# Optimization experiments

Measured on AMD Instinct MI355X. Metric: run time of the kernel, lower is better.

Reference implementation:

```python
import jax, jax.numpy as jnp
import numpy as np

N_NODES = 100000
N_EDGES = 1600000
IN_CH = 64
HID = 64
N_GRAPHS = 64


def _sage_conv(x, src, dst, Wl, bl, Wr, n_nodes):
    # PyG SAGEConv (aggr='mean'): out = lin_l(mean_{j in N(i)} x_j) + lin_r(x_i)
    msg = x[src]                                            # [E, d] gather
    agg = jax.ops.segment_sum(msg, dst, num_segments=n_nodes)
    cnt = jax.ops.segment_sum(jnp.ones((src.shape[0],), x.dtype), dst,
                              num_segments=n_nodes)
    agg = agg / jnp.maximum(cnt, 1.0)[:, None]
    return agg @ Wl + bl + x @ Wr


def setup_inputs() -> dict:
    key = jax.random.key(0)
    ks = jax.random.split(key, 16)
    x = jax.random.normal(ks[0], (N_NODES, IN_CH), jnp.float32)
    edge_index = jax.random.randint(ks[1], (2, N_EDGES), 0, N_NODES, jnp.int64)
    batch = jnp.sort(jax.random.randint(ks[2], (N_NODES,), 0, N_GRAPHS, jnp.int64))

    def glorot(k, fan_in, fan_out):
        s = jnp.sqrt(2.0 / (fan_in + fan_out))
        return jax.random.normal(k, (fan_in, fan_out), jnp.float32) * s

    params = {
        'W1l': glorot(ks[3], IN_CH, HID), 'b1': jnp.zeros((HID,), jnp.float32),
        'W1r': glorot(ks[4], IN_CH, HID),
        'W2l': glorot(ks[5], HID, HID), 'b2': jnp.zeros((HID,), jnp.float32),
        'W2r': glorot(ks[6], HID, HID),
        'W3l': glorot(ks[7], HID, HID), 'b3': jnp.zeros((HID,), jnp.float32),
        'W3r': glorot(ks[8], HID, HID),
        'Wc1': glorot(ks[9], HID, HID // 2), 'bc1': jnp.zeros((HID // 2,), jnp.float32),
        'Wc2': glorot(ks[10], HID // 2, 2), 'bc2': jnp.zeros((2,), jnp.float32),
    }
    return {'x': x, 'edge_index': edge_index, 'batch': batch, **params}


def reference(x, edge_index, batch,
              W1l, b1, W1r, W2l, b2, W2r, W3l, b3, W3r,
              Wc1, bc1, Wc2, bc2):
    src, dst = edge_index[0], edge_index[1]
    n = x.shape[0]
    h = jax.nn.relu(_sage_conv(x, src, dst, W1l, b1, W1r, n))   # dropout = identity (eval)
    h = jax.nn.relu(_sage_conv(h, src, dst, W2l, b2, W2r, n))
    h = jax.nn.relu(_sage_conv(h, src, dst, W3l, b3, W3r, n))
    # global mean pool over graphs
    sums = jax.ops.segment_sum(h, batch, num_segments=N_GRAPHS)
    cnts = jax.ops.segment_sum(jnp.ones((n,), h.dtype), batch, num_segments=N_GRAPHS)
    g = sums / jnp.maximum(cnts, 1.0)[:, None]                  # [G, HID]
    # MLP head (dropout = identity at eval)
    return jax.nn.relu(g @ Wc1 + bc1) @ Wc2 + bc2               # [G, 2]
```

## Files before the change

kernel.cpp:

```cpp
#include <hip/hip_runtime.h>
#include <hip/hip_bf16.h>
#include <hip/hip_fp16.h>

typedef unsigned int u32;
typedef unsigned short u16;
typedef _Float16 f16x8 __attribute__((ext_vector_type(8)));
typedef float f32x4 __attribute__((ext_vector_type(4)));

#define NBLK1 512
#define MMBLK 784

__device__ __forceinline__ u16 f2h(float f) { return __half_as_ushort(__float2half(f)); }
__device__ __forceinline__ u32 packh2(float a, float b) {
    return (u32)f2h(a) | ((u32)f2h(b) << 16);
}
__device__ __forceinline__ __half2 sx(__half2 v, int m) {
    int iv = __shfl_xor(*(int*)&v, m, 64);
    return *(__half2*)&iv;
}

__device__ __forceinline__ int gidx(const void* p, long long i, int w64) {
    if (w64) return (int)((const long long*)p)[i];
    return ((const int*)p)[i];
}

__global__ void init_detect(const int* __restrict__ edge_words, int* __restrict__ flag,
                            u32* __restrict__ ticket, float* __restrict__ pool, int E) {
    const int tid = threadIdx.x;
    for (int i = tid; i < 4096; i += 256) pool[i] = 0.f;
    if (tid == 0) *ticket = 0;
    __shared__ int anyNZ;
    if (tid == 0) anyNZ = 0;
    __syncthreads();
    const long long totalWords = 2LL * E;
    const long long step = totalWords / 1024;
    int nz = 0;
    for (int i = 0; i < 4; ++i) {
        long long w = ((long long)(tid * 4 + i) * step) | 1;
        if (w < totalWords) nz |= edge_words[w];
    }
    if (nz) atomicOr(&anyNZ, 1);
    __syncthreads();
    if (tid == 0) flag[0] = anyNZ ? 0 : 1;
}

__global__ void __launch_bounds__(256) fused_hist_mm1(
        const void* __restrict__ edge, const int* __restrict__ flag,
        u32* __restrict__ HG, int E, int n, int nb1,
        const float* __restrict__ X, const float* __restrict__ Wl,
        const float* __restrict__ Wr, const float* __restrict__ Bv,
        u16* __restrict__ Z, u16* __restrict__ R) {
    if (blockIdx.x < NBLK1) {
        __shared__ u32 h[256];
        const int tid = threadIdx.x;
        h[tid] = 0;
        __syncthreads();
        const int w64 = flag[0];
        const int chunk = (E + NBLK1 - 1) / NBLK1;
        const int s = blockIdx.x * chunk;
        const int e = min(s + chunk, E);
        for (int i = s + tid; i < e; i += 256) {
            int d = gidx(edge, (long long)E + i, w64);
            if ((unsigned)d >= (unsigned)n) d = 0;
            atomicAdd(&h[d >> 9], 1);
        }
        __syncthreads();
        for (int b = tid; b < nb1; b += 256) HG[b * NBLK1 + blockIdx.x] = h[b];
        return;
    }
    const int lane = threadIdx.x & 63;
    const int quad = lane >> 4;
    const int m16 = lane & 15;
    f16x8 bl[2][4], br[2][4];
#pragma unroll
    for (int kh = 0; kh < 2; ++kh)
#pragma unroll
        for (int t = 0; t < 4; ++t)
#pragma unroll
            for (int j = 0; j < 8; ++j) {
                int k = kh * 32 + quad * 8 + j;
                int c = t * 16 + m16;
                bl[kh][t][j] = (_Float16)Wl[k * 64 + c];
                br[kh][t][j] = (_Float16)Wr[k * 64 + c];
            }
    float bias_t[4];
#pragma unroll
    for (int t = 0; t < 4; ++t) bias_t[t] = Bv[t * 16 + m16];

    const int ntiles = (n + 15) >> 4;
    const int nwaves = (gridDim.x - NBLK1) * 4;
    for (int tile = (blockIdx.x - NBLK1) * 4 + (threadIdx.x >> 6); tile < ntiles; tile += nwaves) {
        const int nodeBase = tile << 4;
        int nodeA = nodeBase + m16;
        if (nodeA >= n) nodeA = n - 1;
        f16x8 a[2];
#pragma unroll
        for (int kh = 0; kh < 2; ++kh) {
            const float4* p = (const float4*)(X + (size_t)nodeA * 64 + kh * 32 + quad * 8);
            float4 x0 = p[0], x1 = p[1];
            a[kh][0] = (_Float16)x0.x; a[kh][1] = (_Float16)x0.y;
            a[kh][2] = (_Float16)x0.z; a[kh][3] = (_Float16)x0.w;
            a[kh][4] = (_Float16)x1.x; a[kh][5] = (_Float16)x1.y;
            a[kh][6] = (_Float16)x1.z; a[kh][7] = (_Float16)x1.w;
        }
        f32x4 cl[4], cr[4];
#pragma unroll
        for (int t = 0; t < 4; ++t) {
            f32x4 c0 = {0.f, 0.f, 0.f, 0.f};
            c0 = __builtin_amdgcn_mfma_f32_16x16x32_f16(a[0], bl[0][t], c0, 0, 0, 0);
            c0 = __builtin_amdgcn_mfma_f32_16x16x32_f16(a[1], bl[1][t], c0, 0, 0, 0);
            cl[t] = c0;
            f32x4 c1 = {0.f, 0.f, 0.f, 0.f};
            c1 = __builtin_amdgcn_mfma_f32_16x16x32_f16(a[0], br[0][t], c1, 0, 0, 0);
            c1 = __builtin_amdgcn_mfma_f32_16x16x32_f16(a[1], br[1][t], c1, 0, 0, 0);
            cr[t] = c1;
        }
#pragma unroll
        for (int rg = 0; rg < 4; ++rg) {
            const int node = nodeBase + quad * 4 + rg;
            if (node < n) {
#pragma unroll
                for (int t = 0; t < 4; ++t) {
                    const int c = t * 16 + m16;
                    Z[(size_t)node * 64 + c] = f2h(cl[t][rg]);
                    R[(size_t)node * 64 + c] = f2h(cr[t][rg] + bias_t[t]);
                }
            }
        }
    }
}

__global__ void scanAB(u32* __restrict__ HG, u32* __restrict__ blockSums,
                       u32* __restrict__ SB, u32* __restrict__ ticket, int n) {
    __shared__ u32 ts[256];
    __shared__ int isLast;
    const int ITEMS = 8;
    const int tid = threadIdx.x;
    int base = blockIdx.x * 2048 + tid * ITEMS;
    u32 v[ITEMS];
    u32 sum = 0;
#pragma unroll
    for (int i = 0; i < ITEMS; ++i) {
        int idx = base + i;
        v[i] = (idx < n) ? HG[idx] : 0;
        sum += v[i];
    }
    ts[tid] = sum;
    __syncthreads();
    u32 incl = sum;
    for (int d = 1; d < 256; d <<= 1) {
        u32 y = 0;
        if (tid >= d) y = ts[tid - d];
        __syncthreads();
        incl += y;
        ts[tid] = incl;
        __syncthreads();
    }
    u32 run = incl - sum;
#pragma unroll
    for (int i = 0; i < ITEMS; ++i) {
        int idx = base + i;
        if (idx < n) HG[idx] = run;
        run += v[i];
    }
    if (tid == 255) {
        atomicExch(&blockSums[blockIdx.x], incl);
        __threadfence();
        u32 t = atomicAdd(ticket, 1);
        isLast = (t == gridDim.x - 1);
    }
    __syncthreads();
    if (!isLast) return;
    const int nb = gridDim.x;
    u32 bv = (tid < nb) ? atomicAdd(&blockSums[tid], 0u) : 0;
    ts[tid] = bv;
    __syncthreads();
    u32 bincl = bv;
    for (int d = 1; d < 256; d <<= 1) {
        u32 y = 0;
        if (tid >= d) y = ts[tid - d];
        __syncthreads();
        bincl += y;
        ts[tid] = bincl;
        __syncthreads();
    }
    if (tid < nb) SB[tid] = bincl - bv;
}

__global__ void __launch_bounds__(256) p1_scatter(const void* __restrict__ edge,
                                                  const int* __restrict__ flag,
                                                  const u32* __restrict__ HG,
                                                  const u32* __restrict__ SB,
                                                  u32* __restrict__ P, int E, int n, int nb1) {
    __shared__ u32 base[256];
    __shared__ u32 cur[256];
    const int tid = threadIdx.x;
    cur[tid] = 0;
    for (int b = tid; b < nb1; b += 256) {
        int i = b * NBLK1 + blockIdx.x;
        base[b] = HG[i] + SB[i >> 11];
    }
    __syncthreads();
    const int w64 = flag[0];
    const int chunk = (E + NBLK1 - 1) / NBLK1;
    const int s = blockIdx.x * chunk;
    const int e = min(s + chunk, E);
    for (int i = s + tid; i < e; i += 256) {
        int d = gidx(edge, (long long)E + i, w64);
        if ((unsigned)d >= (unsigned)n) d = 0;
        int sv = gidx(edge, i, w64);
        if ((unsigned)sv >= (unsigned)n) sv = 0;
        const int b1 = d >> 9;
        u32 r = atomicAdd(&cur[b1], 1);
        P[base[b1] + r] = (u32)sv | ((u32)(d & 511) << 17);
    }
}

__global__ void __launch_bounds__(256) p2_kernel(const u32* __restrict__ P,
                                                 const u32* __restrict__ HG,
                                                 const u32* __restrict__ SB,
                                                 u32* __restrict__ offs,
                                                 int* __restrict__ ss, int E, int n, int nb1) {
    __shared__ u32 h2[512];
    __shared__ u32 ts[256];
    const int tid = threadIdx.x;
    const int b = blockIdx.x;
    const int i0 = b * NBLK1;
    const int bs = (int)(HG[i0] + SB[i0 >> 11]);
    int be;
    if (b + 1 < nb1) {
        const int i1 = (b + 1) * NBLK1;
        be = (int)(HG[i1] + SB[i1 >> 11]);
    } else be = E;
    h2[tid] = 0;
    h2[tid + 256] = 0;
    __syncthreads();
    for (int i = bs + tid; i < be; i += 256) atomicAdd(&h2[(P[i] >> 17) & 511], 1);
    __syncthreads();
    u32 v0 = h2[2 * tid], v1 = h2[2 * tid + 1];
    u32 sum = v0 + v1;
    ts[tid] = sum;
    __syncthreads();
    u32 incl = sum;
    for (int d = 1; d < 256; d <<= 1) {
        u32 y = 0;
        if (tid >= d) y = ts[tid - d];
        __syncthreads();
        incl += y;
        ts[tid] = incl;
        __syncthreads();
    }
    u32 run = incl - sum;
    h2[2 * tid] = run;
    h2[2 * tid + 1] = run + v0;
    const int node0 = b * 512 + 2 * tid;
    if (node0 < n) offs[node0] = bs + run;
    if (node0 + 1 < n) offs[node0 + 1] = bs + run + v0;
    if (b == 0 && tid == 0) offs[n] = (u32)E;
    __syncthreads();
    for (int i = bs + tid; i < be; i += 256) {
        u32 p = P[i];
        u32 r = atomicAdd(&h2[(p >> 17) & 511], 1);
        ss[bs + r] = (int)(p & 0x1FFFFu);
    }
}

__global__ void __launch_bounds__(256) mm_mfma_kernel(const u16* __restrict__ X,
                                                      const float* __restrict__ Wl,
                                                      const float* __restrict__ Wr,
                                                      const float* __restrict__ Bv,
                                                      u16* __restrict__ Z,
                                                      u16* __restrict__ R, int n) {
    const int lane = threadIdx.x & 63;
    const int quad = lane >> 4;
    const int m16 = lane & 15;
    f16x8 bl[2][4], br[2][4];
#pragma unroll
    for (int kh = 0; kh < 2; ++kh)
#pragma unroll
        for (int t = 0; t < 4; ++t)
#pragma unroll
            for (int j = 0; j < 8; ++j) {
                int k = kh * 32 + quad * 8 + j;
                int c = t * 16 + m16;
                bl[kh][t][j] = (_Float16)Wl[k * 64 + c];
                br[kh][t][j] = (_Float16)Wr[k * 64 + c];
            }
    float bias_t[4];
#pragma unroll
    for (int t = 0; t < 4; ++t) bias_t[t] = Bv[t * 16 + m16];

    const int ntiles = (n + 15) >> 4;
    const int nwaves = gridDim.x * 4;
    for (int tile = blockIdx.x * 4 + (threadIdx.x >> 6); tile < ntiles; tile += nwaves) {
        const int nodeBase = tile << 4;
        int nodeA = nodeBase + m16;
        if (nodeA >= n) nodeA = n - 1;
        const _Float16* xp = (const _Float16*)X + (size_t)nodeA * 64;
        f16x8 a[2];
#pragma unroll
        for (int kh = 0; kh < 2; ++kh)
            a[kh] = *(const f16x8*)(xp + kh * 32 + quad * 8);
        f32x4 cl[4], cr[4];
#pragma unroll
        for (int t = 0; t < 4; ++t) {
            f32x4 c0 = {0.f, 0.f, 0.f, 0.f};
            c0 = __builtin_amdgcn_mfma_f32_16x16x32_f16(a[0], bl[0][t], c0, 0, 0, 0);
            c0 = __builtin_amdgcn_mfma_f32_16x16x32_f16(a[1], bl[1][t], c0, 0, 0, 0);
            cl[t] = c0;
            f32x4 c1 = {0.f, 0.f, 0.f, 0.f};
            c1 = __builtin_amdgcn_mfma_f32_16x16x32_f16(a[0], br[0][t], c1, 0, 0, 0);
            c1 = __builtin_amdgcn_mfma_f32_16x16x32_f16(a[1], br[1][t], c1, 0, 0, 0);
            cr[t] = c1;
        }
#pragma unroll
        for (int rg = 0; rg < 4; ++rg) {
            const int node = nodeBase + quad * 4 + rg;
            if (node < n) {
#pragma unroll
                for (int t = 0; t < 4; ++t) {
                    const int c = t * 16 + m16;
                    Z[(size_t)node * 64 + c] = f2h(cl[t][rg]);
                    R[(size_t)node * 64 + c] = f2h(cr[t][rg] + bias_t[t]);
                }
            }
        }
    }
}

__global__ void __launch_bounds__(256) agg_kernel(const u16* __restrict__ Zin,
                                                  const u16* __restrict__ Rin,
                                                  const u32* __restrict__ offs,
                                                  const int* __restrict__ ss,
                                                  u16* __restrict__ Hout, int n) {
    const int lane = threadIdx.x & 63;
    const int q = lane >> 4;
    const int sub = lane & 15;
    const u32* Z32 = (const u32*)Zin;
    const int node = (blockIdx.x << 2) | (threadIdx.x >> 6);
    if (node >= n) return;
    const int off = (int)offs[node], end = (int)offs[node + 1];
    const int deg = end - off;
    const __half2 zero2 = __float2half2_rn(0.f);
    const __half2 one2 = __float2half2_rn(1.f);
    __half2 a0 = zero2, a1 = zero2, b0 = zero2, b1 = zero2;
    for (int base = off; base < end; base += 64) {
        const int cnt = min(64, end - base);
        const int idx = ss[base + (lane < cnt ? lane : cnt - 1)];
        const int nb8 = cnt >> 3;
        for (int p = 0; p < nb8; ++p) {
            int j0 = (p << 3) + q;
            int s0 = __shfl(idx, j0, 64);
            int s1 = __shfl(idx, j0 + 4, 64);
            uint2 u0 = *(const uint2*)(Z32 + s0 * 32 + 2 * sub);
            uint2 u1 = *(const uint2*)(Z32 + s1 * 32 + 2 * sub);
            a0 = __hadd2(a0, *(const __half2*)&u0.x);
            a1 = __hadd2(a1, *(const __half2*)&u0.y);
            b0 = __hadd2(b0, *(const __half2*)&u1.x);
            b1 = __hadd2(b1, *(const __half2*)&u1.y);
        }
        const int done = nb8 << 3;
        const int rem = cnt - done;
        if (rem) {
            int j = done + q;
            int s0 = __shfl(idx, j < cnt ? j : cnt - 1, 64);
            uint2 u0 = *(const uint2*)(Z32 + s0 * 32 + 2 * sub);
            __half2 m0 = (j < cnt) ? one2 : zero2;
            a0 = __hfma2(*(const __half2*)&u0.x, m0, a0);
            a1 = __hfma2(*(const __half2*)&u0.y, m0, a1);
            if (rem > 4) {
                int j2 = done + 4 + q;
                int s1 = __shfl(idx, j2 < cnt ? j2 : cnt - 1, 64);
                uint2 u1 = *(const uint2*)(Z32 + s1 * 32 + 2 * sub);
                __half2 m1 = (j2 < cnt) ? one2 : zero2;
                b0 = __hfma2(*(const __half2*)&u1.x, m1, b0);
                b1 = __hfma2(*(const __half2*)&u1.y, m1, b1);
            }
        }
    }
    a0 = __hadd2(a0, b0);
    a1 = __hadd2(a1, b1);
    a0 = __hadd2(a0, sx(a0, 16)); a0 = __hadd2(a0, sx(a0, 32));
    a1 = __hadd2(a1, sx(a1, 16)); a1 = __hadd2(a1, sx(a1, 32));
    if (q == 0) {
        const u32* R32 = (const u32*)Rin;
        uint2 rr = *(const uint2*)(R32 + node * 32 + 2 * sub);
        const float rd = deg > 0 ? 1.f / (float)deg : 0.f;
        float2 s01 = __half22float2(a0);
        float2 s23 = __half22float2(a1);
        float2 r01 = __half22float2(*(const __half2*)&rr.x);
        float2 r23 = __half22float2(*(const __half2*)&rr.y);
        uint2 outp;
        outp.x = packh2(fmaxf(fmaf(s01.x, rd, r01.x), 0.f),
                        fmaxf(fmaf(s01.y, rd, r01.y), 0.f));
        outp.y = packh2(fmaxf(fmaf(s23.x, rd, r23.x), 0.f),
                        fmaxf(fmaf(s23.y, rd, r23.y), 0.f));
        *(uint2*)(((u32*)Hout) + node * 32 + 2 * sub) = outp;
    }
}

__global__ void pool_kernel(const u16* __restrict__ H, const void* __restrict__ batch,
                            const int* __restrict__ flag, float* __restrict__ pool, int n) {
    const int lane = threadIdx.x & 63;
    const int wave = threadIdx.x >> 6;
    int start = (blockIdx.x * 4 + wave) * 64;
    int end = min(start + 64, n);
    if (start >= end) return;
    const int w64 = flag[0];
    float acc = 0.f;
    int cur = gidx(batch, start, w64) & 63;
    for (int i = start; i < end; ++i) {
        int g = gidx(batch, i, w64) & 63;
        if (g != cur) {
            atomicAdd(&pool[cur * 64 + lane], acc);
            acc = 0.f;
            cur = g;
        }
        acc += __half2float(__ushort_as_half(H[i * 64 + lane]));
    }
    atomicAdd(&pool[cur * 64 + lane], acc);
}

__global__ void head_kernel(const float* __restrict__ pool, const void* __restrict__ batch,
                            const int* __restrict__ flag,
                            const float* __restrict__ Wc1, const float* __restrict__ bc1,
                            const float* __restrict__ Wc2, const float* __restrict__ bc2,
                            float* __restrict__ out, int n) {
    __shared__ float gm[64 * 64];
    __shared__ float am[64 * 32];
    __shared__ int cnts[64];
    const int tid = threadIdx.x;
    const int w64 = flag[0];
    if (tid < 64) {
        int lo = 0, hi = n;
        while (lo < hi) { int mid = (lo + hi) >> 1; if (gidx(batch, mid, w64) < tid) lo = mid + 1; else hi = mid; }
        int lo2 = 0, hi2 = n;
        int v2 = tid + 1;
        while (lo2 < hi2) { int mid = (lo2 + hi2) >> 1; if (gidx(batch, mid, w64) < v2) lo2 = mid + 1; else hi2 = mid; }
        cnts[tid] = lo2 - lo;
    }
    __syncthreads();
    for (int i = tid; i < 4096; i += 256) {
        int g = i >> 6;
        float c = (float)(cnts[g] > 0 ? cnts[g] : 1);
        gm[i] = pool[i] / c;
    }
    __syncthreads();
    for (int i = tid; i < 64 * 32; i += 256) {
        int g = i >> 5, j = i & 31;
        float acc = bc1[j];
        for (int k = 0; k < 64; ++k) acc += gm[g * 64 + k] * Wc1[k * 32 + j];
        am[i] = acc > 0.f ? acc : 0.f;
    }
    __syncthreads();
    if (tid < 128) {
        int g = tid >> 1, o = tid & 1;
        float acc = bc2[o];
        for (int j = 0; j < 32; ++j) acc += am[g * 32 + j] * Wc2[j * 2 + o];
        out[tid] = acc;
    }
}

extern "C" void kernel_launch(void* const* d_in, const int* in_sizes, int n_in,
                              void* d_out, int out_size, void* d_ws, size_t ws_size,
                              hipStream_t stream) {
    const float* x   = (const float*)d_in[0];
    const void* edge = d_in[1];
    const void* batch = d_in[2];
    const float* W1l = (const float*)d_in[3];
    const float* b1  = (const float*)d_in[4];
    const float* W1r = (const float*)d_in[5];
    const float* W2l = (const float*)d_in[6];
    const float* b2  = (const float*)d_in[7];
    const float* W2r = (const float*)d_in[8];
    const float* W3l = (const float*)d_in[9];
    const float* b3  = (const float*)d_in[10];
    const float* W3r = (const float*)d_in[11];
    const float* Wc1 = (const float*)d_in[12];
    const float* bc1 = (const float*)d_in[13];
    const float* Wc2 = (const float*)d_in[14];
    const float* bc2 = (const float*)d_in[15];

    const int n = in_sizes[0] / 64;
    const int E = in_sizes[1] / 2;
    const int nb1 = (n + 511) >> 9;
    const int NS = nb1 * NBLK1;

    char* w = (char*)d_ws;
    size_t o = 0;
    auto take = [&](size_t bytes) -> void* {
        void* p = w + o;
        o = (o + bytes + 511) & ~(size_t)511;
        return p;
    };
    int* flag      = (int*)take(sizeof(int));
    u32* ticket    = (u32*)take(sizeof(u32));
    u32* offs      = (u32*)take((size_t)(n + 1) * sizeof(u32));
    u32* HG        = (u32*)take((size_t)(NS + 1) * sizeof(u32));
    u32* blockSums = (u32*)take(256 * sizeof(u32));
    u32* SB        = (u32*)take(256 * sizeof(u32));
    u32* P         = (u32*)take((size_t)E * sizeof(u32));
    int* ss        = (int*)take((size_t)E * sizeof(int));
    u16* Z         = (u16*)take((size_t)n * 64 * sizeof(u16));
    u16* R         = (u16*)take((size_t)n * 64 * sizeof(u16));
    u16* HA        = (u16*)take((size_t)n * 64 * sizeof(u16));
    u16* HB        = (u16*)take((size_t)n * 64 * sizeof(u16));
    float* pool    = (float*)take(64 * 64 * sizeof(float));

    init_detect<<<1, 256, 0, stream>>>((const int*)edge, flag, ticket, pool, E);

    fused_hist_mm1<<<NBLK1 + MMBLK, 256, 0, stream>>>(edge, flag, HG, E, n, nb1,
                                                      x, W1l, W1r, b1, Z, R);
    const int nbScan = (NS + 2047) / 2048;
    scanAB<<<nbScan, 256, 0, stream>>>(HG, blockSums, SB, ticket, NS);
    p1_scatter<<<NBLK1, 256, 0, stream>>>(edge, flag, HG, SB, P, E, n, nb1);
    p2_kernel<<<nb1, 256, 0, stream>>>(P, HG, SB, offs, ss, E, n, nb1);

    const int nodeBlocks = (n + 3) / 4;
    agg_kernel<<<nodeBlocks, 256, 0, stream>>>(Z, R, offs, ss, HA, n);
    mm_mfma_kernel<<<MMBLK, 256, 0, stream>>>(HA, W2l, W2r, b2, Z, R, n);
    agg_kernel<<<nodeBlocks, 256, 0, stream>>>(Z, R, offs, ss, HB, n);
    mm_mfma_kernel<<<MMBLK, 256, 0, stream>>>(HB, W3l, W3r, b3, Z, R, n);
    agg_kernel<<<nodeBlocks, 256, 0, stream>>>(Z, R, offs, ss, HA, n);

    pool_kernel<<<(n + 255) / 256, 256, 0, stream>>>(HA, batch, flag, pool, n);
    head_kernel<<<1, 256, 0, stream>>>(pool, batch, flag, Wc1, bc1, Wc2, bc2,
                                       (float*)d_out, n);
}
```

Baseline: 353.5 us.

## Fold init kernel into others, widen gather unroll, shrink matmul grid

Removes the separate init_detect launch. Each histogram block now detects the 64-bit index width itself, block 0 writes the flag and resets the ticket, and p2_kernel block 0 zeroes the pool buffer. The aggregation kernel gathers four neighbour rows per iteration into eight half2 accumulators instead of two rows into four, to expose more memory-level parallelism. The matmul block count drops from 784 to 256, which relies on mm_mfma_kernel using a grid-stride loop. Width detection now samples fewer words per block and is repeated in 512 blocks.

```diff
diff --git a/kernel.cpp b/kernel.cpp
--- a/kernel.cpp
+++ b/kernel.cpp
@@ -8,7 +8,7 @@
 typedef float f32x4 __attribute__((ext_vector_type(4)));
 
 #define NBLK1 512
-#define MMBLK 784
+#define MMBLK 256
 
 __device__ __forceinline__ u16 f2h(float f) { return __half_as_ushort(__float2half(f)); }
 __device__ __forceinline__ u32 packh2(float a, float b) {
@@ -24,38 +24,32 @@
     return ((const int*)p)[i];
 }
 
-__global__ void init_detect(const int* __restrict__ edge_words, int* __restrict__ flag,
-                            u32* __restrict__ ticket, float* __restrict__ pool, int E) {
-    const int tid = threadIdx.x;
-    for (int i = tid; i < 4096; i += 256) pool[i] = 0.f;
-    if (tid == 0) *ticket = 0;
-    __shared__ int anyNZ;
-    if (tid == 0) anyNZ = 0;
+__device__ __forceinline__ int detect_w64(const int* edge_words, int E, int tid, int* sh) {
+    if (tid == 0) *sh = 0;
     __syncthreads();
     const long long totalWords = 2LL * E;
-    const long long step = totalWords / 1024;
-    int nz = 0;
-    for (int i = 0; i < 4; ++i) {
-        long long w = ((long long)(tid * 4 + i) * step) | 1;
-        if (w < totalWords) nz |= edge_words[w];
-    }
-    if (nz) atomicOr(&anyNZ, 1);
-    __syncthreads();
-    if (tid == 0) flag[0] = anyNZ ? 0 : 1;
+    const long long step = totalWords / 256;
+    long long w = ((long long)tid * step) | 1;
+    int nz = (w < totalWords) ? edge_words[w] : 0;
+    if (nz) atomicOr(sh, 1);
+    __syncthreads();
+    return (*sh) ? 0 : 1;
 }
 
 __global__ void __launch_bounds__(256) fused_hist_mm1(
-        const void* __restrict__ edge, const int* __restrict__ flag,
+        const void* __restrict__ edge, int* __restrict__ flag, u32* __restrict__ ticket,
         u32* __restrict__ HG, int E, int n, int nb1,
         const float* __restrict__ X, const float* __restrict__ Wl,
         const float* __restrict__ Wr, const float* __restrict__ Bv,
         u16* __restrict__ Z, u16* __restrict__ R) {
     if (blockIdx.x < NBLK1) {
         __shared__ u32 h[256];
+        __shared__ int shnz;
         const int tid = threadIdx.x;
         h[tid] = 0;
-        __syncthreads();
-        const int w64 = flag[0];
+        const int w64 = detect_w64((const int*)edge, E, tid, &shnz);
+        if (blockIdx.x == 0 && tid == 0) { flag[0] = w64; *ticket = 0; }
+        __syncthreads();
         const int chunk = (E + NBLK1 - 1) / NBLK1;
         const int s = blockIdx.x * chunk;
         const int e = min(s + chunk, E);
@@ -220,11 +214,15 @@
                                                  const u32* __restrict__ HG,
                                                  const u32* __restrict__ SB,
                                                  u32* __restrict__ offs,
-                                                 int* __restrict__ ss, int E, int n, int nb1) {
+                                                 int* __restrict__ ss,
+                                                 float* __restrict__ pool,
+                                                 int E, int n, int nb1) {
     __shared__ u32 h2[512];
     __shared__ u32 ts[256];
     const int tid = threadIdx.x;
     const int b = blockIdx.x;
+    if (b == 0)
+        for (int i = tid; i < 4096; i += 256) pool[i] = 0.f;
     const int i0 = b * NBLK1;
     const int bs = (int)(HG[i0] + SB[i0 >> 11]);
     int be;
@@ -344,42 +342,60 @@
     const __half2 zero2 = __float2half2_rn(0.f);
     const __half2 one2 = __float2half2_rn(1.f);
     __half2 a0 = zero2, a1 = zero2, b0 = zero2, b1 = zero2;
+    __half2 c0 = zero2, c1 = zero2, d0 = zero2, d1 = zero2;
     for (int base = off; base < end; base += 64) {
         const int cnt = min(64, end - base);
         const int idx = ss[base + (lane < cnt ? lane : cnt - 1)];
-        const int nb8 = cnt >> 3;
-        for (int p = 0; p < nb8; ++p) {
-            int j0 = (p << 3) + q;
+        int p = 0;
+        for (; p + 16 <= cnt; p += 16) {
+            int j0 = p + q;
             int s0 = __shfl(idx, j0, 64);
             int s1 = __shfl(idx, j0 + 4, 64);
+            int s2 = __shfl(idx, j0 + 8, 64);
+            int s3 = __shfl(idx, j0 + 12, 64);
             uint2 u0 = *(const uint2*)(Z32 + s0 * 32 + 2 * sub);
             uint2 u1 = *(const uint2*)(Z32 + s1 * 32 + 2 * sub);
+            uint2 u2 = *(const uint2*)(Z32 + s2 * 32 + 2 * sub);
+            uint2 u3 = *(const uint2*)(Z32 + s3 * 32 + 2 * sub);
             a0 = __hadd2(a0, *(const __half2*)&u0.x);
             a1 = __hadd2(a1, *(const __half2*)&u0.y);
             b0 = __hadd2(b0, *(const __half2*)&u1.x);
             b1 = __hadd2(b1, *(const __half2*)&u1.y);
-        }
-        const int done = nb8 << 3;
-        const int rem = cnt - done;
+            c0 = __hadd2(c0, *(const __half2*)&u2.x);
+            c1 = __hadd2(c1, *(const __half2*)&u2.y);
+            d0 = __hadd2(d0, *(const __half2*)&u3.x);
+            d1 = __hadd2(d1, *(const __half2*)&u3.y);
+        }
+        const int rem = cnt - p;
         if (rem) {
-            int j = done + q;
+            int j = p + q, j1 = p + 4 + q;
             int s0 = __shfl(idx, j < cnt ? j : cnt - 1, 64);
+            int s1 = __shfl(idx, j1 < cnt ? j1 : cnt - 1, 64);
             uint2 u0 = *(const uint2*)(Z32 + s0 * 32 + 2 * sub);
+            uint2 u1 = *(const uint2*)(Z32 + s1 * 32 + 2 * sub);
             __half2 m0 = (j < cnt) ? one2 : zero2;
+            __half2 m1 = (j1 < cnt) ? one2 : zero2;
             a0 = __hfma2(*(const __half2*)&u0.x, m0, a0);
             a1 = __hfma2(*(const __half2*)&u0.y, m0, a1);
-            if (rem > 4) {
-                int j2 = done + 4 + q;
-                int s1 = __shfl(idx, j2 < cnt ? j2 : cnt - 1, 64);
-                uint2 u1 = *(const uint2*)(Z32 + s1 * 32 + 2 * sub);
-                __half2 m1 = (j2 < cnt) ? one2 : zero2;
-                b0 = __hfma2(*(const __half2*)&u1.x, m1, b0);
-                b1 = __hfma2(*(const __half2*)&u1.y, m1, b1);
+            b0 = __hfma2(*(const __half2*)&u1.x, m1, b0);
+            b1 = __hfma2(*(const __half2*)&u1.y, m1, b1);
+            if (rem > 8) {
+                int j2 = p + 8 + q, j3 = p + 12 + q;
+                int s2 = __shfl(idx, j2 < cnt ? j2 : cnt - 1, 64);
+                int s3 = __shfl(idx, j3 < cnt ? j3 : cnt - 1, 64);
+                uint2 u2 = *(const uint2*)(Z32 + s2 * 32 + 2 * sub);
+                uint2 u3 = *(const uint2*)(Z32 + s3 * 32 + 2 * sub);
+                __half2 m2 = (j2 < cnt) ? one2 : zero2;
+                __half2 m3 = (j3 < cnt) ? one2 : zero2;
+                c0 = __hfma2(*(const __half2*)&u2.x, m2, c0);
+                c1 = __hfma2(*(const __half2*)&u2.y, m2, c1);
+                d0 = __hfma2(*(const __half2*)&u3.x, m3, d0);
+                d1 = __hfma2(*(const __half2*)&u3.y, m3, d1);
             }
         }
     }
-    a0 = __hadd2(a0, b0);
-    a1 = __hadd2(a1, b1);
+    a0 = __hadd2(__hadd2(a0, b0), __hadd2(c0, d0));
+    a1 = __hadd2(__hadd2(a1, b1), __hadd2(c1, d1));
     a0 = __hadd2(a0, sx(a0, 16)); a0 = __hadd2(a0, sx(a0, 32));
     a1 = __hadd2(a1, sx(a1, 16)); a1 = __hadd2(a1, sx(a1, 32));
     if (q == 0) {
@@ -507,14 +523,12 @@
     u16* HB        = (u16*)take((size_t)n * 64 * sizeof(u16));
     float* pool    = (float*)take(64 * 64 * sizeof(float));
 
-    init_detect<<<1, 256, 0, stream>>>((const int*)edge, flag, ticket, pool, E);
-
-    fused_hist_mm1<<<NBLK1 + MMBLK, 256, 0, stream>>>(edge, flag, HG, E, n, nb1,
+    fused_hist_mm1<<<NBLK1 + MMBLK, 256, 0, stream>>>(edge, flag, ticket, HG, E, n, nb1,
                                                       x, W1l, W1r, b1, Z, R);
     const int nbScan = (NS + 2047) / 2048;
     scanAB<<<nbScan, 256, 0, stream>>>(HG, blockSums, SB, ticket, NS);
     p1_scatter<<<NBLK1, 256, 0, stream>>>(edge, flag, HG, SB, P, E, n, nb1);
-    p2_kernel<<<nb1, 256, 0, stream>>>(P, HG, SB, offs, ss, E, n, nb1);
+    p2_kernel<<<nb1, 256, 0, stream>>>(P, HG, SB, offs, ss, pool, E, n, nb1);
 
     const int nodeBlocks = (n + 3) / 4;
     agg_kernel<<<nodeBlocks, 256, 0, stream>>>(Z, R, offs, ss, HA, n);
```

Measured after the change: 334.6 us. 1.06x faster.
